# Optimization experiments

Hardware: AMD Instinct MI355X
Metric: run time of the kernel (lower is better)

Reference implementation:

```python
import jax, jax.numpy as jnp
import numpy as np

T, D, E, I, TOP_K = 2048, 2048, 8, 2048, 2
SOFTCAP = 30.0


def setup_inputs() -> dict:
    key = jax.random.key(0)
    ks = jax.random.split(key, 5)
    s = 0.02  # realistic init scale
    return {
        "x": jax.random.normal(ks[0], (T, D), dtype=jnp.float32),
        "w_gate": jax.random.normal(ks[1], (E, D), dtype=jnp.float32) * s,
        "w1": jax.random.normal(ks[2], (E, I, D), dtype=jnp.float32) * s,
        "w3": jax.random.normal(ks[3], (E, I, D), dtype=jnp.float32) * s,
        "w2": jax.random.normal(ks[4], (E, D, I), dtype=jnp.float32) * s,
        "top_k": TOP_K,
    }


def reference(x, w_gate, w1, w3, w2, top_k):
    # Router gating linear in fp32 (ReplicatedLinear, bias=False)
    logits = jnp.einsum("td,ed->te", x.astype(jnp.float32), w_gate)  # [T,E]
    # Softcapped routing logits: cap * tanh(logits / cap)
    logits = SOFTCAP * jnp.tanh(logits / SOFTCAP)
    probs = jax.nn.softmax(logits, axis=-1)                          # [T,E]
    vals, idx = jax.lax.top_k(probs, top_k)                          # [T,k]
    num_experts = w_gate.shape[0]
    # Dense combine weights: zeros except top-k softmax probs (no renorm, Grok-1 style)
    combine = (jax.nn.one_hot(idx, num_experts, dtype=probs.dtype) * vals[..., None]).sum(axis=1)  # [T,E]
    combine = combine.astype(x.dtype)
    # Grok GLU experts: gelu(x@w1^T) * (x@w3^T) @ w2^T, evaluated per expert
    a = jnp.einsum("td,eid->tei", x, w1)  # [T,E,I]
    b = jnp.einsum("td,eid->tei", x, w3)
    h = jax.nn.gelu(a, approximate=False) * b
    y = jnp.einsum("tei,edi->ted", h, w2)  # [T,E,D]
    out = jnp.einsum("te,ted->td", combine, y)
    return out
```

## Files before the change

### kernel.cpp

```cpp
#include <hip/hip_runtime.h>
#include <hip/hip_bf16.h>
#include <math.h>

#define TT 2048
#define DD 2048
#define EE 8
#define II 2048
#define SOFTCAP 30.0f

typedef __attribute__((ext_vector_type(8))) short short8;
typedef __attribute__((ext_vector_type(4))) float f32x4;
typedef unsigned short u16;

__device__ __forceinline__ u16 f2bs(float f) {
    union { __hip_bfloat16 h; u16 u; } cv;
    cv.h = __float2bfloat16(f);
    return cv.u;
}

__device__ __forceinline__ void st_bf4(u16* p, float4 v) {
    unsigned int lo = (unsigned int)f2bs(v.x) | ((unsigned int)f2bs(v.y) << 16);
    unsigned int hi = (unsigned int)f2bs(v.z) | ((unsigned int)f2bs(v.w) << 16);
    *(uint2*)p = make_uint2(lo, hi);
}

__device__ __forceinline__ void gload16(const void* g, void* l) {
    __builtin_amdgcn_global_load_lds(
        (const __attribute__((address_space(1))) unsigned int*)g,
        (__attribute__((address_space(3))) unsigned int*)l,
        16, 0, 0);
}

__global__ __launch_bounds__(256) void cvt_f32_bf16(
    const float* __restrict__ s, u16* __restrict__ d, long long n)
{
    long long i = ((long long)blockIdx.x * 256 + threadIdx.x) * 8;
    if (i >= n) return;
    float4 a = *(const float4*)(s + i);
    float4 b = *(const float4*)(s + i + 4);
    st_bf4(d + i, a);
    st_bf4(d + i + 4, b);
}

__global__ __launch_bounds__(256) void router2_kernel(
    const float* __restrict__ x, const float* __restrict__ wg,
    int* __restrict__ counts, int* __restrict__ list, float* __restrict__ wlist,
    u16* __restrict__ xb)
{
    const int wid = threadIdx.x >> 6;
    const int lane = threadIdx.x & 63;
    const int t = blockIdx.x * 4 + wid;
    const float* xr = x + (size_t)t * DD;
    float acc[EE];
#pragma unroll
    for (int e = 0; e < EE; ++e) acc[e] = 0.f;
    for (int i = 0; i < DD; i += 256) {
        float4 xv = *(const float4*)(xr + i + lane * 4);
        if (xb) st_bf4(xb + (size_t)t * DD + i + lane * 4, xv);
#pragma unroll
        for (int e = 0; e < EE; ++e) {
            float4 wv = *(const float4*)(wg + (size_t)e * DD + i + lane * 4);
            acc[e] += xv.x * wv.x + xv.y * wv.y + xv.z * wv.z + xv.w * wv.w;
        }
    }
#pragma unroll
    for (int e = 0; e < EE; ++e) {
#pragma unroll
        for (int off = 32; off > 0; off >>= 1)
            acc[e] += __shfl_xor(acc[e], off, 64);
    }
    if (lane == 0) {
        float p[EE];
        float mx = -1e30f;
#pragma unroll
        for (int e = 0; e < EE; ++e) {
            p[e] = SOFTCAP * tanhf(acc[e] / SOFTCAP);
            mx = fmaxf(mx, p[e]);
        }
        float s = 0.f;
#pragma unroll
        for (int e = 0; e < EE; ++e) { p[e] = expf(p[e] - mx); s += p[e]; }
        float inv = 1.f / s;
        int i0 = 0;
#pragma unroll
        for (int e = 1; e < EE; ++e) if (p[e] > p[i0]) i0 = e;
        int i1 = (i0 == 0) ? 1 : 0;
#pragma unroll
        for (int e = 0; e < EE; ++e) if (e != i0 && p[e] > p[i1]) i1 = e;
        int pos0 = atomicAdd(&counts[i0], 1);
        list[i0 * TT + pos0] = t * 2;
        wlist[i0 * TT + pos0] = p[i0] * inv;
        int pos1 = atomicAdd(&counts[i1], 1);
        list[i1 * TT + pos1] = t * 2 + 1;
        wlist[i1 * TT + pos1] = p[i1] * inv;
    }
}

__global__ __launch_bounds__(256) void gemm_h_bf16(
    const u16* __restrict__ xb, const u16* __restrict__ w1b,
    const u16* __restrict__ w3b, const int* __restrict__ counts,
    const int* __restrict__ list, const float* __restrict__ wlist,
    u16* __restrict__ H)
{
    const int e = blockIdx.z;
    const int cnt = counts[e];
    const int m0 = blockIdx.y * 128;
    if (m0 >= cnt) return;
    const int n0 = blockIdx.x * 64;
    const int tid = threadIdx.x;
    const int lane = tid & 63;
    const int w = tid >> 6;

    __shared__ u16 As[128 * 32];
    __shared__ u16 W1s[64 * 32];
    __shared__ u16 W3s[64 * 32];

    const int colb = (lane & 3) * 8;
    const int rsub = lane >> 2;
    const int rA0 = w * 16 + rsub;
    const int rA1 = 64 + rA0;
    const int mA0 = m0 + rA0, mA1 = m0 + rA1;
    const int t0 = (mA0 < cnt) ? (list[e * TT + mA0] >> 1) : 0;
    const int t1 = (mA1 < cnt) ? (list[e * TT + mA1] >> 1) : 0;
    const u16* gA0 = xb + (size_t)t0 * DD + colb;
    const u16* gA1 = xb + (size_t)t1 * DD + colb;
    const int rW = w * 16 + rsub;
    const u16* gW1 = w1b + ((size_t)e * II + n0 + rW) * DD + colb;
    const u16* gW3 = w3b + ((size_t)e * II + n0 + rW) * DD + colb;
    u16* lA0 = As + (w * 16) * 32;
    u16* lA1 = As + (64 + w * 16) * 32;
    u16* lW1 = W1s + (w * 16) * 32;
    u16* lW3 = W3s + (w * 16) * 32;

    const int wm = w >> 1, wn = w & 1;
    const int lr = lane & 15;
    const int quad = lane >> 4;

    f32x4 accA[4][2], accB[4][2];
#pragma unroll
    for (int mi = 0; mi < 4; ++mi)
#pragma unroll
        for (int ni = 0; ni < 2; ++ni) {
            accA[mi][ni] = (f32x4)0.f;
            accB[mi][ni] = (f32x4)0.f;
        }

    for (int kk = 0; kk < DD; kk += 32) {
        gload16(gA0 + kk, lA0);
        gload16(gA1 + kk, lA1);
        gload16(gW1 + kk, lW1);
        gload16(gW3 + kk, lW3);
        __syncthreads();

        short8 af[4], b1f[2], b3f[2];
#pragma unroll
        for (int mi = 0; mi < 4; ++mi)
            af[mi] = *(const short8*)&As[(wm * 64 + mi * 16 + lr) * 32 + quad * 8];
#pragma unroll
        for (int ni = 0; ni < 2; ++ni) {
            b1f[ni] = *(const short8*)&W1s[(wn * 32 + ni * 16 + lr) * 32 + quad * 8];
            b3f[ni] = *(const short8*)&W3s[(wn * 32 + ni * 16 + lr) * 32 + quad * 8];
        }
#pragma unroll
        for (int mi = 0; mi < 4; ++mi)
#pragma unroll
            for (int ni = 0; ni < 2; ++ni) {
                accA[mi][ni] = __builtin_amdgcn_mfma_f32_16x16x32_bf16(af[mi], b1f[ni], accA[mi][ni], 0, 0, 0);
                accB[mi][ni] = __builtin_amdgcn_mfma_f32_16x16x32_bf16(af[mi], b3f[ni], accB[mi][ni], 0, 0, 0);
            }
        __syncthreads();
    }

#pragma unroll
    for (int mi = 0; mi < 4; ++mi) {
#pragma unroll
        for (int reg = 0; reg < 4; ++reg) {
            int m = m0 + wm * 64 + mi * 16 + quad * 4 + reg;
            if (m < cnt) {
                int entry = list[e * TT + m];
                float cw = wlist[e * TT + m];
                size_t hbase = (size_t)entry * II;
#pragma unroll
                for (int ni = 0; ni < 2; ++ni) {
                    int col = n0 + wn * 32 + ni * 16 + lr;
                    float a = accA[mi][ni][reg];
                    float b = accB[mi][ni][reg];
                    float g = 0.5f * a * (1.0f + erff(a * 0.70710678118654752f));
                    H[hbase + col] = f2bs(g * b * cw);
                }
            }
        }
    }
}

__global__ __launch_bounds__(256) void gemm_y_bf16(
    const u16* __restrict__ H, const u16* __restrict__ w2b,
    const int* __restrict__ counts, const int* __restrict__ list,
    float* __restrict__ out)
{
    const int e = blockIdx.z;
    const int cnt = counts[e];
    const int m0 = blockIdx.y * 128;
    if (m0 >= cnt) return;
    const int n0 = blockIdx.x * 128;
    const int tid = threadIdx.x;
    const int lane = tid & 63;
    const int w = tid >> 6;

    __shared__ u16 As[128 * 32];
    __shared__ u16 Bs[128 * 32];

    const int colb = (lane & 3) * 8;
    const int rsub = lane >> 2;
    const int rA0 = w * 16 + rsub;
    const int rA1 = 64 + rA0;
    const int eA0 = (m0 + rA0 < cnt) ? list[e * TT + m0 + rA0] : 0;
    const int eA1 = (m0 + rA1 < cnt) ? list[e * TT + m0 + rA1] : 0;
    const u16* gA0 = H + (size_t)eA0 * II + colb;
    const u16* gA1 = H + (size_t)eA1 * II + colb;
    const u16* gB0 = w2b + ((size_t)e * DD + n0 + rA0) * II + colb;
    const u16* gB1 = w2b + ((size_t)e * DD + n0 + rA1) * II + colb;
    u16* lA0 = As + (w * 16) * 32;
    u16* lA1 = As + (64 + w * 16) * 32;
    u16* lB0 = Bs + (w * 16) * 32;
    u16* lB1 = Bs + (64 + w * 16) * 32;

    const int wm = w >> 1, wn = w & 1;
    const int lr = lane & 15;
    const int quad = lane >> 4;

    f32x4 acc[4][4];
#pragma unroll
    for (int mi = 0; mi < 4; ++mi)
#pragma unroll
        for (int ni = 0; ni < 4; ++ni) acc[mi][ni] = (f32x4)0.f;

    for (int kk = 0; kk < II; kk += 32) {
        gload16(gA0 + kk, lA0);
        gload16(gA1 + kk, lA1);
        gload16(gB0 + kk, lB0);
        gload16(gB1 + kk, lB1);
        __syncthreads();

        short8 af[4], bf[4];
#pragma unroll
        for (int mi = 0; mi < 4; ++mi)
            af[mi] = *(const short8*)&As[(wm * 64 + mi * 16 + lr) * 32 + quad * 8];
#pragma unroll
        for (int ni = 0; ni < 4; ++ni)
            bf[ni] = *(const short8*)&Bs[(wn * 64 + ni * 16 + lr) * 32 + quad * 8];
#pragma unroll
        for (int mi = 0; mi < 4; ++mi)
#pragma unroll
            for (int ni = 0; ni < 4; ++ni)
                acc[mi][ni] = __builtin_amdgcn_mfma_f32_16x16x32_bf16(af[mi], bf[ni], acc[mi][ni], 0, 0, 0);
        __syncthreads();
    }

#pragma unroll
    for (int mi = 0; mi < 4; ++mi) {
#pragma unroll
        for (int reg = 0; reg < 4; ++reg) {
            int m = m0 + wm * 64 + mi * 16 + quad * 4 + reg;
            if (m < cnt) {
                int token = list[e * TT + m] >> 1;
                float* orow = out + (size_t)token * DD + n0 + wn * 64;
#pragma unroll
                for (int ni = 0; ni < 4; ++ni)
                    atomicAdd(&orow[ni * 16 + lr], acc[mi][ni][reg]);
            }
        }
    }
}

__global__ __launch_bounds__(256) void gemm_h_fb(
    const float* __restrict__ x, const float* __restrict__ w1,
    const float* __restrict__ w3, const int* __restrict__ counts,
    const int* __restrict__ list, const float* __restrict__ wlist,
    __hip_bfloat16* __restrict__ H)
{
    const int e = blockIdx.z;
    const int cnt = counts[e];
    const int m0 = blockIdx.y * 128;
    if (m0 >= cnt) return;
    const int n0 = blockIdx.x * 64;
    const int tid = threadIdx.x;

    __shared__ u16 As[128][40];
    __shared__ u16 W1s[64][40];
    __shared__ u16 W3s[64][40];

    const int arow = tid >> 1;
    const int ahalf = tid & 1;
    const bool avalid = (m0 + arow) < cnt;
    const float* aptr = nullptr;
    if (avalid) {
        int entry = list[e * TT + m0 + arow];
        aptr = x + (size_t)(entry >> 1) * DD + ahalf * 16;
    }
    const int wrow = tid >> 2;
    const int wq = tid & 3;
    const float* w1ptr = w1 + ((size_t)e * II + (n0 + wrow)) * DD + wq * 8;
    const float* w3ptr = w3 + ((size_t)e * II + (n0 + wrow)) * DD + wq * 8;

    const int lane = tid & 63;
    const int wid = tid >> 6;
    const int wm = wid >> 1;
    const int wn = wid & 1;
    const int lr = lane & 15;
    const int quad = lane >> 4;

    f32x4 accA[4][2], accB[4][2];
#pragma unroll
    for (int mi = 0; mi < 4; ++mi)
#pragma unroll
        for (int ni = 0; ni < 2; ++ni) {
            accA[mi][ni] = (f32x4)0.f;
            accB[mi][ni] = (f32x4)0.f;
        }

    for (int kk = 0; kk < DD; kk += 32) {
#pragma unroll
        for (int it = 0; it < 4; ++it) {
            float4 v = make_float4(0.f, 0.f, 0.f, 0.f);
            if (avalid) v = *(const float4*)(aptr + kk + it * 4);
            st_bf4(&As[arow][ahalf * 16 + it * 4], v);
        }
#pragma unroll
        for (int it = 0; it < 2; ++it) {
            float4 v1 = *(const float4*)(w1ptr + kk + it * 4);
            st_bf4(&W1s[wrow][wq * 8 + it * 4], v1);
            float4 v3 = *(const float4*)(w3ptr + kk + it * 4);
            st_bf4(&W3s[wrow][wq * 8 + it * 4], v3);
        }
        __syncthreads();

        short8 af[4], b1f[2], b3f[2];
#pragma unroll
        for (int mi = 0; mi < 4; ++mi)
            af[mi] = *(const short8*)&As[wm * 64 + mi * 16 + lr][quad * 8];
#pragma unroll
        for (int ni = 0; ni < 2; ++ni) {
            b1f[ni] = *(const short8*)&W1s[wn * 32 + ni * 16 + lr][quad * 8];
            b3f[ni] = *(const short8*)&W3s[wn * 32 + ni * 16 + lr][quad * 8];
        }
#pragma unroll
        for (int mi = 0; mi < 4; ++mi)
#pragma unroll
            for (int ni = 0; ni < 2; ++ni) {
                accA[mi][ni] = __builtin_amdgcn_mfma_f32_16x16x32_bf16(af[mi], b1f[ni], accA[mi][ni], 0, 0, 0);
                accB[mi][ni] = __builtin_amdgcn_mfma_f32_16x16x32_bf16(af[mi], b3f[ni], accB[mi][ni], 0, 0, 0);
            }
        __syncthreads();
    }

#pragma unroll
    for (int mi = 0; mi < 4; ++mi) {
#pragma unroll
        for (int reg = 0; reg < 4; ++reg) {
            int m = m0 + wm * 64 + mi * 16 + quad * 4 + reg;
            if (m < cnt) {
                int entry = list[e * TT + m];
                float cw = wlist[e * TT + m];
                size_t hbase = (size_t)entry * II;
#pragma unroll
                for (int ni = 0; ni < 2; ++ni) {
                    int col = n0 + wn * 32 + ni * 16 + lr;
                    float a = accA[mi][ni][reg];
                    float b = accB[mi][ni][reg];
                    float g = 0.5f * a * (1.0f + erff(a * 0.70710678118654752f));
                    H[hbase + col] = __float2bfloat16(g * b * cw);
                }
            }
        }
    }
}

__global__ __launch_bounds__(256) void gemm_y_fb(
    const __hip_bfloat16* __restrict__ H, const float* __restrict__ w2,
    const int* __restrict__ counts, const int* __restrict__ list,
    float* __restrict__ out)
{
    const int e = blockIdx.z;
    const int cnt = counts[e];
    const int m0 = blockIdx.y * 128;
    if (m0 >= cnt) return;
    const int n0 = blockIdx.x * 128;
    const int tid = threadIdx.x;

    __shared__ u16 As[128][40];
    __shared__ u16 Ws[128][40];

    const int arow = tid >> 1;
    const int ahalf = tid & 1;
    const bool avalid = (m0 + arow) < cnt;
    const u16* aptr = nullptr;
    if (avalid) {
        int entry = list[e * TT + m0 + arow];
        aptr = (const u16*)H + (size_t)entry * II + ahalf * 16;
    }
    const int wrow = tid >> 1;
    const int whalf = tid & 1;
    const float* wptr = w2 + ((size_t)e * DD + (n0 + wrow)) * II + whalf * 16;

    const int lane = tid & 63;
    const int wid = tid >> 6;
    const int wm = wid >> 1;
    const int wn = wid & 1;
    const int lr = lane & 15;
    const int quad = lane >> 4;

    f32x4 acc[4][4];
#pragma unroll
    for (int mi = 0; mi < 4; ++mi)
#pragma unroll
        for (int ni = 0; ni < 4; ++ni) acc[mi][ni] = (f32x4)0.f;

    for (int kk = 0; kk < II; kk += 32) {
#pragma unroll
        for (int it = 0; it < 2; ++it) {
            int4 v = make_int4(0, 0, 0, 0);
            if (avalid) v = *(const int4*)(aptr + kk + it * 8);
            *(int4*)&As[arow][ahalf * 16 + it * 8] = v;
        }
#pragma unroll
        for (int it = 0; it < 4; ++it) {
            float4 v = *(const float4*)(wptr + kk + it * 4);
            st_bf4(&Ws[wrow][whalf * 16 + it * 4], v);
        }
        __syncthreads();

        short8 af[4], bf[4];
#pragma unroll
        for (int mi = 0; mi < 4; ++mi)
            af[mi] = *(const short8*)&As[wm * 64 + mi * 16 + lr][quad * 8];
#pragma unroll
        for (int ni = 0; ni < 4; ++ni)
            bf[ni] = *(const short8*)&Ws[wn * 64 + ni * 16 + lr][quad * 8];
#pragma unroll
        for (int mi = 0; mi < 4; ++mi)
#pragma unroll
            for (int ni = 0; ni < 4; ++ni)
                acc[mi][ni] = __builtin_amdgcn_mfma_f32_16x16x32_bf16(af[mi], bf[ni], acc[mi][ni], 0, 0, 0);
        __syncthreads();
    }

#pragma unroll
    for (int mi = 0; mi < 4; ++mi) {
#pragma unroll
        for (int reg = 0; reg < 4; ++reg) {
            int m = m0 + wm * 64 + mi * 16 + quad * 4 + reg;
            if (m < cnt) {
                int token = list[e * TT + m] >> 1;
                float* orow = out + (size_t)token * DD + n0 + wn * 64;
#pragma unroll
                for (int ni = 0; ni < 4; ++ni)
                    atomicAdd(&orow[ni * 16 + lr], acc[mi][ni][reg]);
            }
        }
    }
}

extern "C" void kernel_launch(void* const* d_in, const int* in_sizes, int n_in,
                              void* d_out, int out_size, void* d_ws, size_t ws_size,
                              hipStream_t stream) {
    const float* x  = (const float*)d_in[0];
    const float* wg = (const float*)d_in[1];
    const float* w1 = (const float*)d_in[2];
    const float* w3 = (const float*)d_in[3];
    const float* w2 = (const float*)d_in[4];
    float* out = (float*)d_out;

    char* ws = (char*)d_ws;
    int*   counts = (int*)(ws);
    int*   list   = (int*)(ws + 4096);
    float* wlist  = (float*)(ws + 4096 + 65536);
    u16*   H      = (u16*)(ws + 135168);
    const size_t NW = (size_t)EE * II * DD;
    u16*   xb  = (u16*)(ws + 135168 + 16777216);
    u16*   w1b = (u16*)((char*)xb + (size_t)TT * DD * 2);
    u16*   w3b = (u16*)((char*)w1b + NW * 2);
    u16*   w2b = (u16*)((char*)w3b + NW * 2);
    const size_t NEED = (size_t)135168 + 16777216 + (size_t)TT * DD * 2 + 3 * NW * 2;

    hipMemsetAsync(counts, 0, EE * sizeof(int), stream);
    hipMemsetAsync(out, 0, (size_t)out_size * sizeof(float), stream);

    if (ws_size >= NEED) {
        router2_kernel<<<TT / 4, 256, 0, stream>>>(x, wg, counts, list, wlist, xb);
        const int cvb = (int)(NW / 8 / 256);
        cvt_f32_bf16<<<cvb, 256, 0, stream>>>(w1, w1b, (long long)NW);
        cvt_f32_bf16<<<cvb, 256, 0, stream>>>(w3, w3b, (long long)NW);
        cvt_f32_bf16<<<cvb, 256, 0, stream>>>(w2, w2b, (long long)NW);
        gemm_h_bf16<<<dim3(II / 64, TT / 128, EE), 256, 0, stream>>>(
            xb, w1b, w3b, counts, list, wlist, H);
        gemm_y_bf16<<<dim3(DD / 128, TT / 128, EE), 256, 0, stream>>>(
            H, w2b, counts, list, out);
    } else {
        router2_kernel<<<TT / 4, 256, 0, stream>>>(x, wg, counts, list, wlist, nullptr);
        gemm_h_fb<<<dim3(II / 64, TT / 128, EE), 256, 0, stream>>>(
            x, w1, w3, counts, list, wlist, (__hip_bfloat16*)H);
        gemm_y_fb<<<dim3(DD / 128, TT / 128, EE), 256, 0, stream>>>(
            (const __hip_bfloat16*)H, w2, counts, list, out);
    }
}
```

Baseline: 690.8 us.

## Double-buffer and swizzle LDS in expert GEMMs, replace output atomics with combine pass

Both bf16 expert GEMMs now use two LDS buffers, so the next K-slice's global-to-LDS loads are issued while the current slice is being multiplied. Both also apply an XOR swizzle on column chunks to reduce LDS bank conflicts on the fragment reads. The second GEMM writes per-(token, slot) rows into a Y scratch buffer that reuses the xb/w1b workspace, instead of atomically adding into out. A new combine kernel then sums the two slots per token, which also removes the output memset. The three weight-conversion launches are merged into one, at the cost of twice the LDS per block and an extra 32MB write and read pass.

```diff
diff --git a/kernel.cpp b/kernel.cpp
--- a/kernel.cpp
+++ b/kernel.cpp
@@ -31,9 +31,16 @@
         16, 0, 0);
 }
 
-__global__ __launch_bounds__(256) void cvt_f32_bf16(
-    const float* __restrict__ s, u16* __restrict__ d, long long n)
-{
+__global__ __launch_bounds__(256) void cvt3_kernel(
+    const float* __restrict__ w1, const float* __restrict__ w3,
+    const float* __restrict__ w2, u16* __restrict__ d1, u16* __restrict__ d3,
+    u16* __restrict__ d2, long long n)
+{
+    const float* s;
+    u16* d;
+    if (blockIdx.y == 0)      { s = w1; d = d1; }
+    else if (blockIdx.y == 1) { s = w3; d = d3; }
+    else                      { s = w2; d = d2; }
     long long i = ((long long)blockIdx.x * 256 + threadIdx.x) * 8;
     if (i >= n) return;
     float4 a = *(const float4*)(s + i);
@@ -95,6 +102,7 @@
         wlist[i1 * TT + pos1] = p[i1] * inv;
     }
 }
+
 
 __global__ __launch_bounds__(256) void gemm_h_bf16(
     const u16* __restrict__ xb, const u16* __restrict__ w1b,
@@ -111,11 +119,11 @@
     const int lane = tid & 63;
     const int w = tid >> 6;
 
-    __shared__ u16 As[128 * 32];
-    __shared__ u16 W1s[64 * 32];
-    __shared__ u16 W3s[64 * 32];
-
-    const int colb = (lane & 3) * 8;
+    __shared__ u16 As[2][128 * 32];
+    __shared__ u16 W1s[2][64 * 32];
+    __shared__ u16 W3s[2][64 * 32];
+
+    const int colb = ((lane & 3) ^ ((lane >> 3) & 3)) * 8;
     const int rsub = lane >> 2;
     const int rA0 = w * 16 + rsub;
     const int rA1 = 64 + rA0;
@@ -127,14 +135,11 @@
     const int rW = w * 16 + rsub;
     const u16* gW1 = w1b + ((size_t)e * II + n0 + rW) * DD + colb;
     const u16* gW3 = w3b + ((size_t)e * II + n0 + rW) * DD + colb;
-    u16* lA0 = As + (w * 16) * 32;
-    u16* lA1 = As + (64 + w * 16) * 32;
-    u16* lW1 = W1s + (w * 16) * 32;
-    u16* lW3 = W3s + (w * 16) * 32;
 
     const int wm = w >> 1, wn = w & 1;
     const int lr = lane & 15;
     const int quad = lane >> 4;
+    const int qc = (quad ^ ((lr >> 1) & 3)) * 8;
 
     f32x4 accA[4][2], accB[4][2];
 #pragma unroll
@@ -145,21 +150,27 @@
             accB[mi][ni] = (f32x4)0.f;
         }
 
-    for (int kk = 0; kk < DD; kk += 32) {
-        gload16(gA0 + kk, lA0);
-        gload16(gA1 + kk, lA1);
-        gload16(gW1 + kk, lW1);
-        gload16(gW3 + kk, lW3);
-        __syncthreads();
+#define STAGE_H(b, kk) do { \
+    gload16(gA0 + (kk), &As[b][(w * 16) * 32]); \
+    gload16(gA1 + (kk), &As[b][(64 + w * 16) * 32]); \
+    gload16(gW1 + (kk), &W1s[b][(w * 16) * 32]); \
+    gload16(gW3 + (kk), &W3s[b][(w * 16) * 32]); \
+} while (0)
+
+    STAGE_H(0, 0);
+    __syncthreads();
+    for (int it = 0; it < DD / 32; ++it) {
+        const int cur = it & 1;
+        if (it + 1 < DD / 32) STAGE_H(cur ^ 1, (it + 1) * 32);
 
         short8 af[4], b1f[2], b3f[2];
 #pragma unroll
         for (int mi = 0; mi < 4; ++mi)
-            af[mi] = *(const short8*)&As[(wm * 64 + mi * 16 + lr) * 32 + quad * 8];
+            af[mi] = *(const short8*)&As[cur][(wm * 64 + mi * 16 + lr) * 32 + qc];
 #pragma unroll
         for (int ni = 0; ni < 2; ++ni) {
-            b1f[ni] = *(const short8*)&W1s[(wn * 32 + ni * 16 + lr) * 32 + quad * 8];
-            b3f[ni] = *(const short8*)&W3s[(wn * 32 + ni * 16 + lr) * 32 + quad * 8];
+            b1f[ni] = *(const short8*)&W1s[cur][(wn * 32 + ni * 16 + lr) * 32 + qc];
+            b3f[ni] = *(const short8*)&W3s[cur][(wn * 32 + ni * 16 + lr) * 32 + qc];
         }
 #pragma unroll
         for (int mi = 0; mi < 4; ++mi)
@@ -170,6 +181,7 @@
             }
         __syncthreads();
     }
+#undef STAGE_H
 
 #pragma unroll
     for (int mi = 0; mi < 4; ++mi) {
@@ -196,7 +208,7 @@
 __global__ __launch_bounds__(256) void gemm_y_bf16(
     const u16* __restrict__ H, const u16* __restrict__ w2b,
     const int* __restrict__ counts, const int* __restrict__ list,
-    float* __restrict__ out)
+    float* __restrict__ Y)
 {
     const int e = blockIdx.z;
     const int cnt = counts[e];
@@ -207,10 +219,10 @@
     const int lane = tid & 63;
     const int w = tid >> 6;
 
-    __shared__ u16 As[128 * 32];
-    __shared__ u16 Bs[128 * 32];
-
-    const int colb = (lane & 3) * 8;
+    __shared__ u16 As[2][128 * 32];
+    __shared__ u16 Bs[2][128 * 32];
+
+    const int colb = ((lane & 3) ^ ((lane >> 3) & 3)) * 8;
     const int rsub = lane >> 2;
     const int rA0 = w * 16 + rsub;
     const int rA1 = 64 + rA0;
@@ -220,14 +232,11 @@
     const u16* gA1 = H + (size_t)eA1 * II + colb;
     const u16* gB0 = w2b + ((size_t)e * DD + n0 + rA0) * II + colb;
     const u16* gB1 = w2b + ((size_t)e * DD + n0 + rA1) * II + colb;
-    u16* lA0 = As + (w * 16) * 32;
-    u16* lA1 = As + (64 + w * 16) * 32;
-    u16* lB0 = Bs + (w * 16) * 32;
-    u16* lB1 = Bs + (64 + w * 16) * 32;
 
     const int wm = w >> 1, wn = w & 1;
     const int lr = lane & 15;
     const int quad = lane >> 4;
+    const int qc = (quad ^ ((lr >> 1) & 3)) * 8;
 
     f32x4 acc[4][4];
 #pragma unroll
@@ -235,20 +244,26 @@
 #pragma unroll
         for (int ni = 0; ni < 4; ++ni) acc[mi][ni] = (f32x4)0.f;
 
-    for (int kk = 0; kk < II; kk += 32) {
-        gload16(gA0 + kk, lA0);
-        gload16(gA1 + kk, lA1);
-        gload16(gB0 + kk, lB0);
-        gload16(gB1 + kk, lB1);
-        __syncthreads();
+#define STAGE_Y(b, kk) do { \
+    gload16(gA0 + (kk), &As[b][(w * 16) * 32]); \
+    gload16(gA1 + (kk), &As[b][(64 + w * 16) * 32]); \
+    gload16(gB0 + (kk), &Bs[b][(w * 16) * 32]); \
+    gload16(gB1 + (kk), &Bs[b][(64 + w * 16) * 32]); \
+} while (0)
+
+    STAGE_Y(0, 0);
+    __syncthreads();
+    for (int it = 0; it < II / 32; ++it) {
+        const int cur = it & 1;
+        if (it + 1 < II / 32) STAGE_Y(cur ^ 1, (it + 1) * 32);
 
         short8 af[4], bf[4];
 #pragma unroll
         for (int mi = 0; mi < 4; ++mi)
-            af[mi] = *(const short8*)&As[(wm * 64 + mi * 16 + lr) * 32 + quad * 8];
+            af[mi] = *(const short8*)&As[cur][(wm * 64 + mi * 16 + lr) * 32 + qc];
 #pragma unroll
         for (int ni = 0; ni < 4; ++ni)
-            bf[ni] = *(const short8*)&Bs[(wn * 64 + ni * 16 + lr) * 32 + quad * 8];
+            bf[ni] = *(const short8*)&Bs[cur][(wn * 64 + ni * 16 + lr) * 32 + qc];
 #pragma unroll
         for (int mi = 0; mi < 4; ++mi)
 #pragma unroll
@@ -256,6 +271,7 @@
                 acc[mi][ni] = __builtin_amdgcn_mfma_f32_16x16x32_bf16(af[mi], bf[ni], acc[mi][ni], 0, 0, 0);
         __syncthreads();
     }
+#undef STAGE_Y
 
 #pragma unroll
     for (int mi = 0; mi < 4; ++mi) {
@@ -263,14 +279,26 @@
         for (int reg = 0; reg < 4; ++reg) {
             int m = m0 + wm * 64 + mi * 16 + quad * 4 + reg;
             if (m < cnt) {
-                int token = list[e * TT + m] >> 1;
-                float* orow = out + (size_t)token * DD + n0 + wn * 64;
+                int entry = list[e * TT + m];
+                float* yrow = Y + (size_t)entry * DD + n0 + wn * 64;
 #pragma unroll
                 for (int ni = 0; ni < 4; ++ni)
-                    atomicAdd(&orow[ni * 16 + lr], acc[mi][ni][reg]);
+                    yrow[ni * 16 + lr] = acc[mi][ni][reg];
             }
         }
     }
+}
+
+__global__ __launch_bounds__(256) void combine_kernel(
+    const float* __restrict__ Y, float* __restrict__ out)
+{
+    long long i4 = ((long long)blockIdx.x * 256 + threadIdx.x) * 4;
+    int t = (int)(i4 >> 11);
+    int d = (int)(i4 & 2047);
+    float4 a = *(const float4*)(Y + (size_t)(2 * t) * DD + d);
+    float4 b = *(const float4*)(Y + (size_t)(2 * t + 1) * DD + d);
+    float4 r = make_float4(a.x + b.x, a.y + b.y, a.z + b.z, a.w + b.w);
+    *(float4*)(out + i4) = r;
 }
 
 __global__ __launch_bounds__(256) void gemm_h_fb(
@@ -481,22 +509,22 @@
     u16*   w1b = (u16*)((char*)xb + (size_t)TT * DD * 2);
     u16*   w3b = (u16*)((char*)w1b + NW * 2);
     u16*   w2b = (u16*)((char*)w3b + NW * 2);
+    float* Y = (float*)xb;
     const size_t NEED = (size_t)135168 + 16777216 + (size_t)TT * DD * 2 + 3 * NW * 2;
 
     hipMemsetAsync(counts, 0, EE * sizeof(int), stream);
-    hipMemsetAsync(out, 0, (size_t)out_size * sizeof(float), stream);
 
     if (ws_size >= NEED) {
         router2_kernel<<<TT / 4, 256, 0, stream>>>(x, wg, counts, list, wlist, xb);
         const int cvb = (int)(NW / 8 / 256);
-        cvt_f32_bf16<<<cvb, 256, 0, stream>>>(w1, w1b, (long long)NW);
-        cvt_f32_bf16<<<cvb, 256, 0, stream>>>(w3, w3b, (long long)NW);
-        cvt_f32_bf16<<<cvb, 256, 0, stream>>>(w2, w2b, (long long)NW);
+        cvt3_kernel<<<dim3(cvb, 3), 256, 0, stream>>>(w1, w3, w2, w1b, w3b, w2b, (long long)NW);
         gemm_h_bf16<<<dim3(II / 64, TT / 128, EE), 256, 0, stream>>>(
             xb, w1b, w3b, counts, list, wlist, H);
         gemm_y_bf16<<<dim3(DD / 128, TT / 128, EE), 256, 0, stream>>>(
-            H, w2b, counts, list, out);
+            H, w2b, counts, list, Y);
+        combine_kernel<<<(TT * DD / 4) / 256, 256, 0, stream>>>(Y, out);
     } else {
+        hipMemsetAsync(out, 0, (size_t)out_size * sizeof(float), stream);
         router2_kernel<<<TT / 4, 256, 0, stream>>>(x, wg, counts, list, wlist, nullptr);
         gemm_h_fb<<<dim3(II / 64, TT / 128, EE), 256, 0, stream>>>(
             x, w1, w3, counts, list, wlist, (__hip_bfloat16*)H);
```

After: 677.2 us. 2.0% less time.
